# Kernel tuning notes

Measured on AMD Instinct MI355X. Metric: run time of the kernel, lower is better.

Reference implementation:

```python
import jax, jax.numpy as jnp
import numpy as np

N_NODES = 100000
N_EDGES = 1600000


def setup_inputs() -> dict:
    key = jax.random.key(0)
    ks = jax.random.split(key, 16)
    d_emb, d_mlp, d_lstm = 128, 256, 256
    B, C, T = 8, 4, 128
    return {
        "input_ids": jax.random.randint(ks[0], (B, C, T), 0, N_NODES, dtype=jnp.int64 if jax.config.jax_enable_x64 else jnp.int32),
        "input_mask": jnp.ones((B, C, T), dtype=jnp.int32),
        "labels": jax.random.uniform(ks[1], (B, C), dtype=jnp.float32),
        "src": jax.random.randint(ks[2], (N_EDGES,), 0, N_NODES),
        "dst": jax.random.randint(ks[3], (N_EDGES,), 0, N_NODES),
        "edge_value": jax.random.uniform(ks[4], (N_EDGES,), dtype=jnp.float32),
        "node_emb": jax.random.normal(ks[5], (N_NODES, d_emb), dtype=jnp.float32),
        "W1": jax.random.normal(ks[6], (d_mlp, d_emb), dtype=jnp.float32) * 0.05,
        "b1": jax.random.normal(ks[7], (d_mlp,), dtype=jnp.float32) * 0.05,
        "w_ih": jax.random.normal(ks[8], (4 * d_lstm, d_mlp), dtype=jnp.float32) * 0.05,
        "w_hh": jax.random.normal(ks[9], (4 * d_lstm, d_lstm), dtype=jnp.float32) * 0.05,
        "b_ih": jax.random.normal(ks[10], (4 * d_lstm,), dtype=jnp.float32) * 0.05,
        "b_hh": jax.random.normal(ks[11], (4 * d_lstm,), dtype=jnp.float32) * 0.05,
        "W2": jax.random.normal(ks[12], (1, d_lstm), dtype=jnp.float32) * 0.05,
        "b2": jax.random.normal(ks[13], (1,), dtype=jnp.float32) * 0.05,
    }


def reference(input_ids, input_mask, labels, src, dst, edge_value,
              node_emb, W1, b1, w_ih, w_hh, b_ih, b_hh, W2, b2):
    N = node_emb.shape[0]
    # edge-weighted mean message passing: u_mul_e('embedding','value') -> mean
    m = node_emb[src] * edge_value[:, None]                       # [E, d_emb]
    agg = jax.ops.segment_sum(m, dst, num_segments=N)             # [N, d_emb]
    cnt = jax.ops.segment_sum(jnp.ones_like(edge_value), dst, num_segments=N)
    h_nodes = agg / jnp.maximum(cnt, 1.0)[:, None]
    # linear1 on all nodes
    t_nodes = h_nodes @ W1.T + b1                                  # [N, d_mlp]
    B, C, T = input_ids.shape
    x = t_nodes[input_ids.reshape(B * C, T)]                       # [BC, T, d_mlp]
    lengths = input_mask.sum(axis=-1).reshape(B * C)               # [BC]
    H = w_hh.shape[1]

    def step(carry, xt):
        h, c = carry
        gates = xt @ w_ih.T + b_ih + h @ w_hh.T + b_hh
        i, f, g, o = jnp.split(gates, 4, axis=-1)  # torch LSTM gate order
        c = jax.nn.sigmoid(f) * c + jax.nn.sigmoid(i) * jnp.tanh(g)
        h = jax.nn.sigmoid(o) * jnp.tanh(c)
        return (h, c), h

    h0 = jnp.zeros((B * C, H), x.dtype)
    _, hs = jax.lax.scan(step, (h0, h0), jnp.swapaxes(x, 0, 1))    # [T, BC, H]
    hs = jnp.swapaxes(hs, 0, 1)                                    # [BC, T, H]
    idx = (lengths - 1).astype(jnp.int32)[:, None, None]
    h_last = jnp.take_along_axis(hs, jnp.broadcast_to(idx, (B * C, 1, H)), axis=1)[:, 0, :]
    scores = (h_last @ W2.T + b2).reshape(B, C)                    # [B, 4]
    p = jax.nn.softmax(scores, axis=1)
    # BCEWithLogits applied to softmaxed scores (as in the original)
    error = jnp.mean(jnp.maximum(p, 0) - p * labels + jnp.log1p(jnp.exp(-jnp.abs(p))))
    predictions = jnp.argmax(p, axis=1)
    return error, predictions
```

## Files before the change

kernel.cpp:

```cpp
#include <hip/hip_runtime.h>
#include <math.h>

#define NNODES 100000
#define NEDGES 1600000
#define NPOS   4096
#define NSEQ   32
#define TSTEPS 128

typedef float f32x4 __attribute__((ext_vector_type(4)));
typedef unsigned u32x4 __attribute__((ext_vector_type(4)));
typedef _Float16 h2v __attribute__((ext_vector_type(2)));

#define OFF_SLOT   0
#define OFF_AGG    400128
#define OFF_CNT    2497280
#define OFF_WF     2513664
#define OFF_BIASF  3037952
#define OFF_PREG   3042048
#define OFF_HS     19819264
#define OFF_WH16A  OFF_AGG
#define OFF_WH16L  (OFF_AGG + 192 * 512 * 4)

static __device__ __forceinline__ float fdot2(unsigned w, unsigned h, float acc) {
#if __has_builtin(__builtin_amdgcn_fdot2)
  h2v wv, hv;
  __builtin_memcpy(&wv, &w, 4);
  __builtin_memcpy(&hv, &h, 4);
  return __builtin_amdgcn_fdot2(wv, hv, acc, false);
#else
  asm("v_dot2_f32_f16 %0, %1, %2, %0" : "+v"(acc) : "v"(w), "v"(h));
  return acc;
#endif
}

__global__ void k_init(int* slotmap, float* agg, float* cnt, float* hs0) {
  int i = blockIdx.x * blockDim.x + threadIdx.x;
  int stride = gridDim.x * blockDim.x;
  for (int idx = i; idx < 4096 * 128; idx += stride) agg[idx] = 0.f;
  for (int idx = i; idx < NNODES; idx += stride) slotmap[idx] = -1;
  for (int idx = i; idx < 4096; idx += stride) cnt[idx] = 0.f;
  for (int idx = i; idx < 8192; idx += stride) hs0[idx] = 0.f;
}

__global__ void k_mark(const int* __restrict__ input_ids, int* __restrict__ slotmap) {
  int p = blockIdx.x * blockDim.x + threadIdx.x;
  if (p < NPOS) atomicCAS(&slotmap[input_ids[p]], -1, p);
}

__global__ void k_edge(const int* __restrict__ src, const int* __restrict__ dst,
                       const float* __restrict__ ev, const float* __restrict__ emb,
                       const int* __restrict__ slotmap,
                       float* __restrict__ agg, float* __restrict__ cnt) {
  int e = blockIdx.x * 256 + threadIdx.x;
  int lane = threadIdx.x & 63;
  int d = dst[e];
  int slot = slotmap[d];
  int sn = 0; float vv = 0.f;
  if (slot >= 0) { sn = src[e]; vv = ev[e]; }
  unsigned long long m = __ballot(slot >= 0);
  while (m) {
    int j = __ffsll(m) - 1;
    m &= m - 1;
    int sl = __shfl(slot, j);
    int s2 = __shfl(sn, j);
    float v = __shfl(vv, j);
    float2 em = *(const float2*)&emb[(size_t)s2 * 128 + 2 * lane];
    atomicAdd(&agg[sl * 128 + 2 * lane],     em.x * v);
    atomicAdd(&agg[sl * 128 + 2 * lane + 1], em.y * v);
    if (lane == 0) atomicAdd(&cnt[sl], 1.f);
  }
}

__global__ void k_div(float* __restrict__ agg, const float* __restrict__ cnt) {
  int i = blockIdx.x * blockDim.x + threadIdx.x;
  agg[i] /= fmaxf(cnt[i >> 7], 1.f);
}

__global__ void k_fuse(const float* __restrict__ w_ih, const float* __restrict__ W1,
                       const float* __restrict__ b1, const float* __restrict__ b_ih,
                       const float* __restrict__ b_hh,
                       float* __restrict__ Wf, float* __restrict__ bf) {
  int row = blockIdx.x;
  int e = threadIdx.x;
  float acc = 0.f;
  for (int m2 = 0; m2 < 256; ++m2) acc += w_ih[row * 256 + m2] * W1[m2 * 128 + e];
  Wf[row * 128 + e] = acc;
  if (e == 0) {
    float bacc = b_ih[row] + b_hh[row];
    for (int m2 = 0; m2 < 256; ++m2) bacc += w_ih[row * 256 + m2] * b1[m2];
    bf[row] = bacc;
  }
}

__global__ __launch_bounds__(256, 2) void k_pregemm(
    const float* __restrict__ hnode, const float* __restrict__ Wf,
    const float* __restrict__ bf, const int* __restrict__ slotmap,
    const int* __restrict__ input_ids, float* __restrict__ preg) {
  __shared__ float Ash[64][132];
  __shared__ float Bsh[64][132];
  __shared__ int slots[64];
  int tid = threadIdx.x;
  int bm = (blockIdx.x & 63) * 64;
  int bn = (blockIdx.x >> 6) * 64;
  if (tid < 64) slots[tid] = slotmap[input_ids[bm + tid]];
  __syncthreads();
#pragma unroll
  for (int i = 0; i < 8; ++i) {
    int idx = tid + 256 * i;
    int r = idx >> 5, c = idx & 31;
    *(float4*)&Ash[r][c * 4] = *(const float4*)&hnode[slots[r] * 128 + c * 4];
    *(float4*)&Bsh[r][c * 4] = *(const float4*)&Wf[(bn + r) * 128 + c * 4];
  }
  __syncthreads();
  int tx = tid & 15, ty = tid >> 4;
  float acc[4][4] = {};
  for (int k = 0; k < 128; k += 4) {
    float4 a[4], bb[4];
#pragma unroll
    for (int i = 0; i < 4; ++i) a[i] = *(const float4*)&Ash[tx + 16 * i][k];
#pragma unroll
    for (int j = 0; j < 4; ++j) bb[j] = *(const float4*)&Bsh[ty + 16 * j][k];
#pragma unroll
    for (int i = 0; i < 4; ++i)
#pragma unroll
      for (int j = 0; j < 4; ++j)
        acc[i][j] += a[i].x * bb[j].x + a[i].y * bb[j].y + a[i].z * bb[j].z + a[i].w * bb[j].w;
  }
#pragma unroll
  for (int j = 0; j < 4; ++j) {
    int row = bn + ty + 16 * j;
    float bias = bf[row];
    int q  = row >> 8;
    int mm = (row >> 5) & 7;
    int dl = row & 31;
#pragma unroll
    for (int i = 0; i < 4; ++i) {
      int p = bm + tx + 16 * i;
      int s = p >> 7, tt = p & 127;
      preg[(((size_t)(tt * 32 + s) * 8 + mm) * 4 + q) * 32 + dl] = acc[i][j] + bias;
    }
  }
}

__global__ void k_wcvt(const float* __restrict__ w_hh,
                       unsigned* __restrict__ wA, unsigned* __restrict__ wL) {
  int idx = blockIdx.x * 256 + threadIdx.x;
  int row = idx >> 7;
  int j   = idx & 127;
  float x0 = w_hh[(size_t)row * 256 + 2 * j];
  float x1 = w_hh[(size_t)row * 256 + 2 * j + 1];
  union { _Float16 f[2]; unsigned u; } pk;
  pk.f[0] = (_Float16)x0;
  pk.f[1] = (_Float16)x1;
  int q = row >> 8, d = row & 255;
  int kseg = j >> 6, jj = j & 63;
  int tid = kseg * 256 + d;
  if (q < 3) {
    wA[(q * 64 + jj) * 512 + tid] = pk.u;
  } else {
    wL[((jj >> 2) * 512 + tid) * 4 + (jj & 3)] = pk.u;
  }
}

__global__ __launch_bounds__(512, 1) void k_lstm(
    const unsigned* __restrict__ wh16A, const unsigned* __restrict__ wh16L,
    const float* __restrict__ preg, float* __restrict__ hs) {
  __shared__ __align__(16) unsigned whL[16 * 512 * 4];
  __shared__ __align__(16) unsigned h16[128];
  __shared__ __align__(16) float    accb[256 * 4];
  const int tid  = threadIdx.x;
  const int s    = blockIdx.x;
  const int kseg = tid >> 8;
  const int d    = tid & 255;
  const bool owner = (kseg == 0);

  unsigned wv[192];
  {
    const unsigned* wa = wh16A + tid;
#pragma unroll
    for (int e = 0; e < 192; ++e) wv[e] = wa[e * 512];
#pragma unroll
    for (int i = 0; i < 16; ++i)
      *(u32x4*)&whL[(i * 512 + tid) * 4] = *(const u32x4*)&wh16L[(i * 512 + tid) * 4];
  }
  if (tid < 128) h16[tid] = 0u;
  float c_st = 0.f;
  __syncthreads();

  const float* pregs = preg + ((size_t)s * 8 + (d >> 5)) * 128 + (d & 31);

  for (int t = 0; t < TSTEPS; ++t) {
    float pg0 = 0.f, pg1 = 0.f, pg2 = 0.f, pg3 = 0.f;
    if (owner) {
      const float* pb = pregs + (size_t)t * 32768;
      pg0 = pb[0]; pg1 = pb[32]; pg2 = pb[64]; pg3 = pb[96];
    }
    float a0 = 0.f, a1 = 0.f, a2 = 0.f, a3 = 0.f;
    const unsigned* hseg = h16 + kseg * 64;
#pragma unroll
    for (int c = 0; c < 16; ++c) {
      u32x4 h4 = *(const u32x4*)(hseg + c * 4);
      u32x4 w3 = *(const u32x4*)&whL[(c * 512 + tid) * 4];
#pragma unroll
      for (int k = 0; k < 4; ++k) {
        a0 = fdot2(wv[0 * 64 + c * 4 + k], h4[k], a0);
        a1 = fdot2(wv[1 * 64 + c * 4 + k], h4[k], a1);
        a2 = fdot2(wv[2 * 64 + c * 4 + k], h4[k], a2);
        a3 = fdot2(w3[k],                  h4[k], a3);
      }
    }
    if (!owner) {
      f32x4 r; r.x = a0; r.y = a1; r.z = a2; r.w = a3;
      *(f32x4*)&accb[d * 4] = r;
    }
    __syncthreads();
    if (owner) {
      f32x4 r = *(const f32x4*)&accb[d * 4];
      float gi = a0 + r.x + pg0;
      float gf = a1 + r.y + pg1;
      float gg = a2 + r.z + pg2;
      float go = a3 + r.w + pg3;
      float si = 1.f / (1.f + expf(-gi));
      float sf = 1.f / (1.f + expf(-gf));
      float so = 1.f / (1.f + expf(-go));
      float cc = sf * c_st + si * tanhf(gg);
      float hh = so * tanhf(cc);
      c_st = cc;
      ((_Float16*)h16)[d] = (_Float16)hh;
      hs[(size_t)(t + 1) * 8192 + s * 256 + d] = hh;
    }
    __syncthreads();
  }
}

__global__ void k_final(const float* __restrict__ hs, const int* __restrict__ mask,
                        const float* __restrict__ labels, const float* __restrict__ W2,
                        const float* __restrict__ b2, float* __restrict__ out) {
  __shared__ float scores[32];
  __shared__ float errpart[8];
  int tid = threadIdx.x;
  if (tid < 32) {
    int len = 0;
    for (int t = 0; t < 128; ++t) len += mask[tid * 128 + t];
    if (len < 1) len = 1;
    const float* hl = hs + (size_t)len * 8192 + tid * 256;
    float acc = b2[0];
    for (int k = 0; k < 256; ++k) acc += hl[k] * W2[k];
    scores[tid] = acc;
  }
  __syncthreads();
  if (tid < 8) {
    float sc[4];
#pragma unroll
    for (int i = 0; i < 4; ++i) sc[i] = scores[tid * 4 + i];
    float mx = fmaxf(fmaxf(sc[0], sc[1]), fmaxf(sc[2], sc[3]));
    float ex[4], ssum = 0.f;
#pragma unroll
    for (int i = 0; i < 4; ++i) { ex[i] = expf(sc[i] - mx); ssum += ex[i]; }
    float esum = 0.f; int am = 0; float best = -1e30f;
#pragma unroll
    for (int i = 0; i < 4; ++i) {
      float p = ex[i] / ssum;
      float li = labels[tid * 4 + i];
      esum += fmaxf(p, 0.f) - p * li + log1pf(expf(-fabsf(p)));
      if (p > best) { best = p; am = i; }
    }
    errpart[tid] = esum;
    out[1 + tid] = (float)am;
  }
  __syncthreads();
  if (tid == 0) {
    float e = 0.f;
    for (int i = 0; i < 8; ++i) e += errpart[i];
    out[0] = e / 32.f;
  }
}

extern "C" void kernel_launch(void* const* d_in, const int* in_sizes, int n_in,
                              void* d_out, int out_size, void* d_ws, size_t ws_size,
                              hipStream_t stream) {
  const int*   input_ids  = (const int*)d_in[0];
  const int*   input_mask = (const int*)d_in[1];
  const float* labels     = (const float*)d_in[2];
  const int*   src        = (const int*)d_in[3];
  const int*   dst        = (const int*)d_in[4];
  const float* ev         = (const float*)d_in[5];
  const float* node_emb   = (const float*)d_in[6];
  const float* W1         = (const float*)d_in[7];
  const float* b1         = (const float*)d_in[8];
  const float* w_ih       = (const float*)d_in[9];
  const float* w_hh       = (const float*)d_in[10];
  const float* b_ih       = (const float*)d_in[11];
  const float* b_hh       = (const float*)d_in[12];
  const float* W2         = (const float*)d_in[13];
  const float* b2         = (const float*)d_in[14];
  float* out = (float*)d_out;
  char* ws = (char*)d_ws;
  int*      slotmap = (int*)(ws + OFF_SLOT);
  float*    agg     = (float*)(ws + OFF_AGG);
  float*    cnt     = (float*)(ws + OFF_CNT);
  float*    Wf      = (float*)(ws + OFF_WF);
  float*    biasf   = (float*)(ws + OFF_BIASF);
  float*    preg    = (float*)(ws + OFF_PREG);
  float*    hs      = (float*)(ws + OFF_HS);
  unsigned* wh16A   = (unsigned*)(ws + OFF_WH16A);
  unsigned* wh16L   = (unsigned*)(ws + OFF_WH16L);

  hipLaunchKernelGGL(k_init,    dim3(2048), dim3(256), 0, stream, slotmap, agg, cnt, hs);
  hipLaunchKernelGGL(k_mark,    dim3(16),   dim3(256), 0, stream, input_ids, slotmap);
  hipLaunchKernelGGL(k_edge,    dim3(6250), dim3(256), 0, stream, src, dst, ev, node_emb, slotmap, agg, cnt);
  hipLaunchKernelGGL(k_div,     dim3(2048), dim3(256), 0, stream, agg, cnt);
  hipLaunchKernelGGL(k_fuse,    dim3(1024), dim3(128), 0, stream, w_ih, W1, b1, b_ih, b_hh, Wf, biasf);
  hipLaunchKernelGGL(k_pregemm, dim3(1024), dim3(256), 0, stream, agg, Wf, biasf, slotmap, input_ids, preg);
  hipLaunchKernelGGL(k_wcvt,    dim3(512),  dim3(256), 0, stream, w_hh, wh16A, wh16L);
  hipLaunchKernelGGL(k_lstm,    dim3(NSEQ), dim3(512), 0, stream, wh16A, wh16L, preg, hs);
  hipLaunchKernelGGL(k_final,   dim3(1),    dim3(64),  0, stream, hs, input_mask, labels, W2, b2, out);
}
```

Measured before the change: 337.4 us.

## Split LSTM recurrent dot-products across four K-segments with 1024 threads

The recurrent matvec in the LSTM kernel now uses 1024 threads per sequence, each covering 32 of the 128 packed fp16 pairs instead of 64. Each thread keeps 92 weight words in registers, with the rest of the g gate and the o gate in LDS. The shared reduction buffer grows to hold three partial sums that the owner thread adds. This halves the serial fdot2 chain per step and spreads the weights over more registers, at the cost of more LDS reduction traffic, wider barriers and a harder register budget.

```diff
diff --git a/kernel.cpp b/kernel.cpp
--- a/kernel.cpp
+++ b/kernel.cpp
@@ -6,6 +6,7 @@
 #define NPOS   4096
 #define NSEQ   32
 #define TSTEPS 128
+#define WRES   92
 
 typedef float f32x4 __attribute__((ext_vector_type(4)));
 typedef unsigned u32x4 __attribute__((ext_vector_type(4)));
@@ -19,7 +20,7 @@
 #define OFF_PREG   3042048
 #define OFF_HS     19819264
 #define OFF_WH16A  OFF_AGG
-#define OFF_WH16L  (OFF_AGG + 192 * 512 * 4)
+#define OFF_WH16L  (OFF_AGG + WRES * 1024 * 4)
 
 static __device__ __forceinline__ float fdot2(unsigned w, unsigned h, float acc) {
 #if __has_builtin(__builtin_amdgcn_fdot2)
@@ -143,7 +144,7 @@
 }
 
 __global__ void k_wcvt(const float* __restrict__ w_hh,
-                       unsigned* __restrict__ wA, unsigned* __restrict__ wL) {
+                       unsigned* __restrict__ wRo, unsigned* __restrict__ wLo) {
   int idx = blockIdx.x * 256 + threadIdx.x;
   int row = idx >> 7;
   int j   = idx & 127;
@@ -152,42 +153,51 @@
   union { _Float16 f[2]; unsigned u; } pk;
   pk.f[0] = (_Float16)x0;
   pk.f[1] = (_Float16)x1;
-  int q = row >> 8, d = row & 255;
-  int kseg = j >> 6, jj = j & 63;
-  int tid = kseg * 256 + d;
-  if (q < 3) {
-    wA[(q * 64 + jj) * 512 + tid] = pk.u;
+  int q = row >> 8, dd = row & 255;
+  int kseg = j >> 5, p = j & 31;
+  int tid = kseg * 256 + dd;
+  if (q < 2) {
+    wRo[(q * 32 + p) * 1024 + tid] = pk.u;
+  } else if (q == 2 && p < 28) {
+    wRo[(64 + p) * 1024 + tid] = pk.u;
+  } else if (q == 2) {
+    wLo[(0 * 1024 + tid) * 4 + (p - 28)] = pk.u;
   } else {
-    wL[((jj >> 2) * 512 + tid) * 4 + (jj & 3)] = pk.u;
-  }
-}
-
-__global__ __launch_bounds__(512, 1) void k_lstm(
-    const unsigned* __restrict__ wh16A, const unsigned* __restrict__ wh16L,
+    wLo[((1 + (p >> 2)) * 1024 + tid) * 4 + (p & 3)] = pk.u;
+  }
+}
+
+__global__ __launch_bounds__(1024) void k_lstm(
+    const unsigned* __restrict__ wR, const unsigned* __restrict__ wLg,
     const float* __restrict__ preg, float* __restrict__ hs) {
-  __shared__ __align__(16) unsigned whL[16 * 512 * 4];
+  __shared__ __align__(16) unsigned whL[9 * 1024 * 4];
   __shared__ __align__(16) unsigned h16[128];
-  __shared__ __align__(16) float    accb[256 * 4];
+  __shared__ __align__(16) float    accb[3 * 256 * 4];
   const int tid  = threadIdx.x;
   const int s    = blockIdx.x;
   const int kseg = tid >> 8;
   const int d    = tid & 255;
   const bool owner = (kseg == 0);
 
-  unsigned wv[192];
+  unsigned wv[WRES];
   {
-    const unsigned* wa = wh16A + tid;
-#pragma unroll
-    for (int e = 0; e < 192; ++e) wv[e] = wa[e * 512];
-#pragma unroll
-    for (int i = 0; i < 16; ++i)
-      *(u32x4*)&whL[(i * 512 + tid) * 4] = *(const u32x4*)&wh16L[(i * 512 + tid) * 4];
+    const unsigned* wa = wR + tid;
+#pragma unroll
+    for (int e = 0; e < WRES; ++e) wv[e] = wa[e * 1024];
+#pragma unroll
+    for (int e = 0; e < WRES; ++e) asm volatile("" : "+v"(wv[e]));
+    const u32x4* srcL = (const u32x4*)wLg;
+    u32x4* dstL = (u32x4*)whL;
+#pragma unroll
+    for (int j = 0; j < 9; ++j) dstL[j * 1024 + tid] = srcL[j * 1024 + tid];
   }
   if (tid < 128) h16[tid] = 0u;
   float c_st = 0.f;
   __syncthreads();
 
   const float* pregs = preg + ((size_t)s * 8 + (d >> 5)) * 128 + (d & 31);
+  const u32x4* Lb   = (const u32x4*)whL + tid;
+  const u32x4* hseg = (const u32x4*)h16 + kseg * 8;
 
   for (int t = 0; t < TSTEPS; ++t) {
     float pg0 = 0.f, pg1 = 0.f, pg2 = 0.f, pg3 = 0.f;
@@ -196,30 +206,32 @@
       pg0 = pb[0]; pg1 = pb[32]; pg2 = pb[64]; pg3 = pb[96];
     }
     float a0 = 0.f, a1 = 0.f, a2 = 0.f, a3 = 0.f;
-    const unsigned* hseg = h16 + kseg * 64;
-#pragma unroll
-    for (int c = 0; c < 16; ++c) {
-      u32x4 h4 = *(const u32x4*)(hseg + c * 4);
-      u32x4 w3 = *(const u32x4*)&whL[(c * 512 + tid) * 4];
+    u32x4 g2t = Lb[0];
+#pragma unroll
+    for (int c = 0; c < 8; ++c) {
+      u32x4 h4 = hseg[c];
+      u32x4 w3 = Lb[(1 + c) * 1024];
 #pragma unroll
       for (int k = 0; k < 4; ++k) {
-        a0 = fdot2(wv[0 * 64 + c * 4 + k], h4[k], a0);
-        a1 = fdot2(wv[1 * 64 + c * 4 + k], h4[k], a1);
-        a2 = fdot2(wv[2 * 64 + c * 4 + k], h4[k], a2);
-        a3 = fdot2(w3[k],                  h4[k], a3);
+        a0 = fdot2(wv[c * 4 + k],      h4[k], a0);
+        a1 = fdot2(wv[32 + c * 4 + k], h4[k], a1);
+        a2 = fdot2(c < 7 ? wv[64 + c * 4 + k] : g2t[k], h4[k], a2);
+        a3 = fdot2(w3[k],              h4[k], a3);
       }
     }
     if (!owner) {
       f32x4 r; r.x = a0; r.y = a1; r.z = a2; r.w = a3;
-      *(f32x4*)&accb[d * 4] = r;
+      *(f32x4*)&accb[((kseg - 1) * 256 + d) * 4] = r;
     }
     __syncthreads();
     if (owner) {
-      f32x4 r = *(const f32x4*)&accb[d * 4];
-      float gi = a0 + r.x + pg0;
-      float gf = a1 + r.y + pg1;
-      float gg = a2 + r.z + pg2;
-      float go = a3 + r.w + pg3;
+      f32x4 r0 = *(const f32x4*)&accb[(0 * 256 + d) * 4];
+      f32x4 r1 = *(const f32x4*)&accb[(1 * 256 + d) * 4];
+      f32x4 r2 = *(const f32x4*)&accb[(2 * 256 + d) * 4];
+      float gi = a0 + r0.x + r1.x + r2.x + pg0;
+      float gf = a1 + r0.y + r1.y + r2.y + pg1;
+      float gg = a2 + r0.z + r1.z + r2.z + pg2;
+      float go = a3 + r0.w + r1.w + r2.w + pg3;
       float si = 1.f / (1.f + expf(-gi));
       float sf = 1.f / (1.f + expf(-gf));
       float so = 1.f / (1.f + expf(-go));
@@ -306,13 +318,13 @@
   unsigned* wh16A   = (unsigned*)(ws + OFF_WH16A);
   unsigned* wh16L   = (unsigned*)(ws + OFF_WH16L);
 
-  hipLaunchKernelGGL(k_init,    dim3(2048), dim3(256), 0, stream, slotmap, agg, cnt, hs);
-  hipLaunchKernelGGL(k_mark,    dim3(16),   dim3(256), 0, stream, input_ids, slotmap);
-  hipLaunchKernelGGL(k_edge,    dim3(6250), dim3(256), 0, stream, src, dst, ev, node_emb, slotmap, agg, cnt);
-  hipLaunchKernelGGL(k_div,     dim3(2048), dim3(256), 0, stream, agg, cnt);
-  hipLaunchKernelGGL(k_fuse,    dim3(1024), dim3(128), 0, stream, w_ih, W1, b1, b_ih, b_hh, Wf, biasf);
-  hipLaunchKernelGGL(k_pregemm, dim3(1024), dim3(256), 0, stream, agg, Wf, biasf, slotmap, input_ids, preg);
-  hipLaunchKernelGGL(k_wcvt,    dim3(512),  dim3(256), 0, stream, w_hh, wh16A, wh16L);
-  hipLaunchKernelGGL(k_lstm,    dim3(NSEQ), dim3(512), 0, stream, wh16A, wh16L, preg, hs);
-  hipLaunchKernelGGL(k_final,   dim3(1),    dim3(64),  0, stream, hs, input_mask, labels, W2, b2, out);
-}
+  hipLaunchKernelGGL(k_init,    dim3(2048), dim3(256),  0, stream, slotmap, agg, cnt, hs);
+  hipLaunchKernelGGL(k_mark,    dim3(16),   dim3(256),  0, stream, input_ids, slotmap);
+  hipLaunchKernelGGL(k_edge,    dim3(6250), dim3(256),  0, stream, src, dst, ev, node_emb, slotmap, agg, cnt);
+  hipLaunchKernelGGL(k_div,     dim3(2048), dim3(256),  0, stream, agg, cnt);
+  hipLaunchKernelGGL(k_fuse,    dim3(1024), dim3(128),  0, stream, w_ih, W1, b1, b_ih, b_hh, Wf, biasf);
+  hipLaunchKernelGGL(k_pregemm, dim3(1024), dim3(256),  0, stream, agg, Wf, biasf, slotmap, input_ids, preg);
+  hipLaunchKernelGGL(k_wcvt,    dim3(512),  dim3(256),  0, stream, w_hh, wh16A, wh16L);
+  hipLaunchKernelGGL(k_lstm,    dim3(NSEQ), dim3(1024), 0, stream, wh16A, wh16L, preg, hs);
+  hipLaunchKernelGGL(k_final,   dim3(1),    dim3(64),   0, stream, hs, input_mask, labels, W2, b2, out);
+}
```

Measured after the change: 334.9 us. About the same (-0.8%).
